# Kernel optimization log

Hardware: AMD Instinct MI355X
Metric: run time of the kernel (lower is better)

## Reference

```python
import jax, jax.numpy as jnp
import numpy as np

N_NODES = 100000
N_EDGES = 1600000
IN_FEAT = 128
HID_FEAT = 128
OUT_FEAT = 128


def setup_inputs() -> dict:
    key = jax.random.key(0)
    k1, k2, k3, k4, k5 = jax.random.split(key, 5)
    x = jax.random.normal(k1, (N_NODES, IN_FEAT), dtype=jnp.float32)
    # Xavier-ish scale for weights
    W_in = jax.random.normal(k2, (2, IN_FEAT, HID_FEAT), dtype=jnp.float32) * (1.0 / np.sqrt(IN_FEAT))
    W_out = jax.random.normal(k3, (2, HID_FEAT, OUT_FEAT), dtype=jnp.float32) * (1.0 / np.sqrt(HID_FEAT))
    src = jax.random.randint(k4, (N_EDGES,), 0, N_NODES, dtype=jnp.int32)
    dst = jax.random.randint(k5, (N_EDGES,), 0, N_NODES, dtype=jnp.int32)
    return {"x": x, "W_in": W_in, "W_out": W_out, "src": src, "dst": dst}


def _mean_aggregate(h, src, dst, num_nodes):
    # copy_src('h','m') + fn.mean('m','neigh'): gather src feats, segment-mean by dst.
    msgs = h[src]                                             # [E, D]
    summed = jax.ops.segment_sum(msgs, dst, num_segments=num_nodes)   # [N, D]
    deg = jax.ops.segment_sum(jnp.ones((src.shape[0],), h.dtype), dst,
                              num_segments=num_nodes)         # [N]
    deg = jnp.maximum(deg, 1.0)                               # zero-in-degree -> 0 output
    return summed / deg[:, None]


def reference(x, W_in, W_out, src, dst):
    n = x.shape[0]
    # Layer 0 (i == 0): uses weight_in, ReLU activation (i != K-1)
    neigh = _mean_aggregate(x, src, dst, n)
    h = x @ W_in[0] + neigh @ W_in[1]
    h = jax.nn.relu(h)
    # Layer 1 (i == K-1): uses weight_out, no activation
    neigh = _mean_aggregate(h, src, dst, n)
    h = h @ W_out[0] + neigh @ W_out[1]
    return h
```

## Files before the change

### kernel.cpp

```cpp
#include <hip/hip_runtime.h>

#define NF 128
#define NBSHIFT 8
#define NBMAX 512
#define CHUNK 4096

typedef __attribute__((ext_vector_type(8))) short bf16x8;
typedef __attribute__((ext_vector_type(4))) float f32x4;
typedef __attribute__((ext_vector_type(2))) float f32x2;

__device__ __forceinline__ unsigned short f2bf(float f) {
    unsigned int u = __builtin_bit_cast(unsigned int, f);
    u = (u + 0x7fffu + ((u >> 16) & 1u)) >> 16;
    return (unsigned short)u;
}
__device__ __forceinline__ float bflo(unsigned int u) {
    return __builtin_bit_cast(float, u << 16);
}
__device__ __forceinline__ float bfhi(unsigned int u) {
    return __builtin_bit_cast(float, u & 0xffff0000u);
}
__device__ __forceinline__ unsigned char f2fp8(float v) {
    return (unsigned char)(__builtin_amdgcn_cvt_pk_fp8_f32(v, v, 0, false) & 0xff);
}

#define BH 256
#define BT 256
__global__ __launch_bounds__(256) void k_prep(const int* __restrict__ dst, int E, int NB,
                                              int* __restrict__ gbhist,
                                              const float* __restrict__ x,
                                              unsigned short* __restrict__ xb,
                                              unsigned char* __restrict__ xq,
                                              const float* __restrict__ Win,
                                              const float* __restrict__ Wout,
                                              unsigned short* __restrict__ BtIn,
                                              unsigned short* __restrict__ BtOut) {
    __shared__ int lh[NBMAX];
    const int bb = blockIdx.x;
    const int t = threadIdx.x;
    if (bb < BH) {
        for (int k = t; k < NBMAX; k += 256) lh[k] = 0;
        __syncthreads();
        for (int i = bb * 256 + t; i < E; i += BH * 256)
            atomicAdd(&lh[((unsigned)dst[i]) >> NBSHIFT], 1);
        __syncthreads();
        for (int k = t; k < NB; k += 256)
            if (lh[k]) atomicAdd(&gbhist[k], lh[k]);
    } else if (bb < BH + BT) {
        int b2 = bb - BH;
        const float* W = (b2 < 128) ? Win : Wout;
        unsigned short* Bt = (b2 < 128) ? BtIn : BtOut;
        int idx = (b2 & 127) * 256 + t;
        int c = idx >> 8;
        int k = idx & 255;
        int p = k >> 7, kk = k & 127;
        Bt[idx] = f2bf(W[((size_t)p * NF + kk) * NF + c]);
    } else {
        long long i = (long long)(bb - BH - BT) * 256 + t;
        const float4 a = *reinterpret_cast<const float4*>(x + i * 8);
        const float4 b = *reinterpret_cast<const float4*>(x + i * 8 + 4);
        union { unsigned short s[8]; uint4 u; } o;
        o.s[0] = f2bf(a.x); o.s[1] = f2bf(a.y); o.s[2] = f2bf(a.z); o.s[3] = f2bf(a.w);
        o.s[4] = f2bf(b.x); o.s[5] = f2bf(b.y); o.s[6] = f2bf(b.z); o.s[7] = f2bf(b.w);
        *reinterpret_cast<uint4*>(xb + i * 8) = o.u;
        int lo = __builtin_amdgcn_cvt_pk_fp8_f32(a.x, a.y, 0, false);
        lo = __builtin_amdgcn_cvt_pk_fp8_f32(a.z, a.w, lo, true);
        int hi = __builtin_amdgcn_cvt_pk_fp8_f32(b.x, b.y, 0, false);
        hi = __builtin_amdgcn_cvt_pk_fp8_f32(b.z, b.w, hi, true);
        uint2 oq; oq.x = (unsigned)lo; oq.y = (unsigned)hi;
        *reinterpret_cast<uint2*>(xq + i * 8) = oq;
    }
}


__global__ __launch_bounds__(256) void k_bscan(const int* __restrict__ gbhist,
                                               int* __restrict__ bbase, int* __restrict__ gcursor,
                                               int NB, int E, int* __restrict__ offsets, int n) {
    __shared__ int sA[NBMAX], sB[NBMAX];
    int t = threadIdx.x;
    for (int k = t; k < NBMAX; k += 256) sA[k] = (k < NB) ? gbhist[k] : 0;
    __syncthreads();
    int* pin = sA;
    int* pout = sB;
    for (int off = 1; off < NBMAX; off <<= 1) {
        for (int k = t; k < NBMAX; k += 256) pout[k] = pin[k] + (k >= off ? pin[k - off] : 0);
        __syncthreads();
        int* tmp = pin; pin = pout; pout = tmp;
    }
    for (int k = t; k < NB; k += 256) {
        int excl = pin[k] - gbhist[k];
        bbase[k] = excl;
        gcursor[k] = excl;
    }
    if (t == 0) {
        bbase[NB] = E;
        offsets[n] = E;
    }
}

__global__ __launch_bounds__(256) void k_bucket(const int* __restrict__ src,
                                                const int* __restrict__ dst,
                                                int* __restrict__ gcursor,
                                                unsigned* __restrict__ gpairs, int E) {
    __shared__ int lhist[NBMAX], lbase[NBMAX], lcur[NBMAX], gb[NBMAX];
    __shared__ int sA[NBMAX], sB[NBMAX];
    __shared__ unsigned stage[CHUNK];
    __shared__ unsigned short stage_b[CHUNK];
    const int t = threadIdx.x;
    const int c0 = blockIdx.x * CHUNK;
    const int cc = min(CHUNK, E - c0);

    for (int k = t; k < NBMAX; k += 256) lhist[k] = 0;
    __syncthreads();

    int ls[16], ld[16];
#pragma unroll
    for (int j = 0; j < 16; ++j) {
        int i = t + j * 256;
        ls[j] = 0; ld[j] = 0;
        if (i < cc) {
            ls[j] = src[c0 + i];
            ld[j] = dst[c0 + i];
            atomicAdd(&lhist[((unsigned)ld[j]) >> NBSHIFT], 1);
        }
    }
    __syncthreads();
    for (int k = t; k < NBMAX; k += 256) sA[k] = lhist[k];
    __syncthreads();
    int* pin = sA;
    int* pout = sB;
    for (int off = 1; off < NBMAX; off <<= 1) {
        for (int k = t; k < NBMAX; k += 256) pout[k] = pin[k] + (k >= off ? pin[k - off] : 0);
        __syncthreads();
        int* tmp = pin; pin = pout; pout = tmp;
    }
    for (int k = t; k < NBMAX; k += 256) {
        int excl = pin[k] - lhist[k];
        lbase[k] = excl;
        lcur[k] = excl;
        int cnt = lhist[k];
        if (cnt > 0) gb[k] = atomicAdd(&gcursor[k], cnt);
    }
    __syncthreads();
#pragma unroll
    for (int j = 0; j < 16; ++j) {
        int i = t + j * 256;
        if (i < cc) {
            int b = ((unsigned)ld[j]) >> NBSHIFT;
            int pos = atomicAdd(&lcur[b], 1);
            stage[pos] = (((unsigned)ld[j] & 255u) << 24) | (unsigned)ls[j];
            stage_b[pos] = (unsigned short)b;
        }
    }
    __syncthreads();
    for (int idx = t; idx < cc; idx += 256) {
        unsigned p = stage[idx];
        int b = stage_b[idx];
        gpairs[gb[b] + (idx - lbase[b])] = p;
    }
}

__global__ __launch_bounds__(256) void k_bsort(const unsigned* __restrict__ gpairs,
                                               const int* __restrict__ bbase,
                                               int* __restrict__ offsets,
                                               float* __restrict__ invdeg,
                                               int* __restrict__ esrc, int n) {
    __shared__ int lcnt[256], lcur[256], sA[256], sB[256];
    const int b = blockIdx.x;
    const int t = threadIdx.x;
    const int base = bbase[b];
    const int c = bbase[b + 1] - base;
    const int n0 = b << NBSHIFT;

    lcnt[t] = 0;
    __syncthreads();
    for (int i = t; i < c; i += 256) {
        int node = (int)(gpairs[base + i] >> 24);
        atomicAdd(&lcnt[node], 1);
    }
    __syncthreads();
    sA[t] = lcnt[t];
    __syncthreads();
    int* pin = sA;
    int* pout = sB;
    for (int off = 1; off < 256; off <<= 1) {
        pout[t] = pin[t] + (t >= off ? pin[t - off] : 0);
        __syncthreads();
        int* tmp = pin; pin = pout; pout = tmp;
    }
    int excl = pin[t] - lcnt[t];
    lcur[t] = excl;
    int node_g = n0 + t;
    if (node_g < n) {
        offsets[node_g] = base + excl;
        invdeg[node_g] = 1.0f / (float)max(lcnt[t], 1);
    }
    __syncthreads();
    for (int i = t; i < c; i += 256) {
        unsigned p = gpairs[base + i];
        int node = (int)(p >> 24);
        int pos = atomicAdd(&lcur[node], 1);
        esrc[base + pos] = (int)(p & 0x00ffffffu);
    }
}

__global__ __launch_bounds__(256) void k_agg_fp8(const unsigned char* __restrict__ feat,
                                                 const int* __restrict__ esrc,
                                                 const int* __restrict__ offsets,
                                                 const float* __restrict__ invdeg,
                                                 unsigned short* __restrict__ neigh, int n) {
    int wid0 = (int)(((long long)blockIdx.x * blockDim.x + threadIdx.x) >> 6);
    const int wid = __builtin_amdgcn_readfirstlane(wid0);
    if (wid >= n) return;
    const int lane = threadIdx.x & 63;
    const int g = lane >> 4;
    const int q = lane & 15;
    const unsigned qoff = (unsigned)q * 8u;
    const unsigned char* fb = feat;

    const int beg = offsets[wid];
    const int end = offsets[wid + 1];
    f32x2 c01 = {0.f, 0.f}, c23 = {0.f, 0.f}, c45 = {0.f, 0.f}, c67 = {0.f, 0.f};

    int i = beg;
    for (; i + 16 <= end; i += 16) {
        int e[16];
#pragma unroll
        for (int j = 0; j < 16; ++j) e[j] = esrc[i + j];
#pragma unroll
        for (int u = 0; u < 4; ++u) {
            int es = (g & 2) ? ((g & 1) ? e[u * 4 + 3] : e[u * 4 + 2])
                             : ((g & 1) ? e[u * 4 + 1] : e[u * 4 + 0]);
            uint2 v = *(const uint2*)(fb + (unsigned)es * 128u + qoff);
            c01 += __builtin_amdgcn_cvt_pk_f32_fp8((int)v.x, false);
            c23 += __builtin_amdgcn_cvt_pk_f32_fp8((int)v.x, true);
            c45 += __builtin_amdgcn_cvt_pk_f32_fp8((int)v.y, false);
            c67 += __builtin_amdgcn_cvt_pk_f32_fp8((int)v.y, true);
        }
    }
    for (; i + 4 <= end; i += 4) {
        int e0 = esrc[i + 0], e1 = esrc[i + 1], e2 = esrc[i + 2], e3 = esrc[i + 3];
        int es = (g & 2) ? ((g & 1) ? e3 : e2) : ((g & 1) ? e1 : e0);
        uint2 v = *(const uint2*)(fb + (unsigned)es * 128u + qoff);
        c01 += __builtin_amdgcn_cvt_pk_f32_fp8((int)v.x, false);
        c23 += __builtin_amdgcn_cvt_pk_f32_fp8((int)v.x, true);
        c45 += __builtin_amdgcn_cvt_pk_f32_fp8((int)v.y, false);
        c67 += __builtin_amdgcn_cvt_pk_f32_fp8((int)v.y, true);
    }
    if (i < end) {
        int r = end - i;
        if (g < r) {
            int es = esrc[i + g];
            uint2 v = *(const uint2*)(fb + (unsigned)es * 128u + qoff);
            c01 += __builtin_amdgcn_cvt_pk_f32_fp8((int)v.x, false);
            c23 += __builtin_amdgcn_cvt_pk_f32_fp8((int)v.x, true);
            c45 += __builtin_amdgcn_cvt_pk_f32_fp8((int)v.y, false);
            c67 += __builtin_amdgcn_cvt_pk_f32_fp8((int)v.y, true);
        }
    }
    float a0 = c01.x, a1 = c01.y, a2 = c23.x, a3 = c23.y;
    float a4 = c45.x, a5 = c45.y, a6 = c67.x, a7 = c67.y;
    a0 += __shfl_xor(a0, 16); a1 += __shfl_xor(a1, 16);
    a2 += __shfl_xor(a2, 16); a3 += __shfl_xor(a3, 16);
    a4 += __shfl_xor(a4, 16); a5 += __shfl_xor(a5, 16);
    a6 += __shfl_xor(a6, 16); a7 += __shfl_xor(a7, 16);
    a0 += __shfl_xor(a0, 32); a1 += __shfl_xor(a1, 32);
    a2 += __shfl_xor(a2, 32); a3 += __shfl_xor(a3, 32);
    a4 += __shfl_xor(a4, 32); a5 += __shfl_xor(a5, 32);
    a6 += __shfl_xor(a6, 32); a7 += __shfl_xor(a7, 32);

    const float sc = invdeg[wid];
    a0 *= sc; a1 *= sc; a2 *= sc; a3 *= sc;
    a4 *= sc; a5 *= sc; a6 *= sc; a7 *= sc;
    unsigned p0, p1, p2, p3;
    asm("v_cvt_pk_bf16_f32 %0, %1, %2" : "=v"(p0) : "v"(a0), "v"(a1));
    asm("v_cvt_pk_bf16_f32 %0, %1, %2" : "=v"(p1) : "v"(a2), "v"(a3));
    asm("v_cvt_pk_bf16_f32 %0, %1, %2" : "=v"(p2) : "v"(a4), "v"(a5));
    asm("v_cvt_pk_bf16_f32 %0, %1, %2" : "=v"(p3) : "v"(a6), "v"(a7));
    if (g == 0) {
        uint4 o; o.x = p0; o.y = p1; o.z = p2; o.w = p3;
        *(uint4*)((char*)neigh + (size_t)wid * 256 + (unsigned)q * 16u) = o;
    }
}

__global__ __launch_bounds__(256) void k_agg_bf16(const unsigned short* __restrict__ feat,
                                                  const int* __restrict__ esrc,
                                                  const int* __restrict__ offsets,
                                                  const float* __restrict__ invdeg,
                                                  unsigned short* __restrict__ neigh, int n) {
    int wid0 = (int)(((long long)blockIdx.x * blockDim.x + threadIdx.x) >> 6);
    const int wid = __builtin_amdgcn_readfirstlane(wid0);
    if (wid >= n) return;
    const int lane = threadIdx.x & 63;
    const int g = lane >> 4;
    const int q = lane & 15;
    const unsigned qoff = (unsigned)q * 16u;
    const char* fb = (const char*)feat;
    const int beg = offsets[wid];
    const int end = offsets[wid + 1];
    float a0 = 0.f, a1 = 0.f, a2 = 0.f, a3 = 0.f, a4 = 0.f, a5 = 0.f, a6 = 0.f, a7 = 0.f;
    int i = beg;
    for (; i + 4 <= end; i += 4) {
        int e0 = esrc[i + 0], e1 = esrc[i + 1], e2 = esrc[i + 2], e3 = esrc[i + 3];
        int es = (g & 2) ? ((g & 1) ? e3 : e2) : ((g & 1) ? e1 : e0);
        uint4 v = *(const uint4*)(fb + (unsigned)es * 256u + qoff);
        a0 += bflo(v.x); a1 += bfhi(v.x);
        a2 += bflo(v.y); a3 += bfhi(v.y);
        a4 += bflo(v.z); a5 += bfhi(v.z);
        a6 += bflo(v.w); a7 += bfhi(v.w);
    }
    if (i < end) {
        int r = end - i;
        if (g < r) {
            int es = esrc[i + g];
            uint4 v = *(const uint4*)(fb + (unsigned)es * 256u + qoff);
            a0 += bflo(v.x); a1 += bfhi(v.x);
            a2 += bflo(v.y); a3 += bfhi(v.y);
            a4 += bflo(v.z); a5 += bfhi(v.z);
            a6 += bflo(v.w); a7 += bfhi(v.w);
        }
    }
    a0 += __shfl_xor(a0, 16); a1 += __shfl_xor(a1, 16);
    a2 += __shfl_xor(a2, 16); a3 += __shfl_xor(a3, 16);
    a4 += __shfl_xor(a4, 16); a5 += __shfl_xor(a5, 16);
    a6 += __shfl_xor(a6, 16); a7 += __shfl_xor(a7, 16);
    a0 += __shfl_xor(a0, 32); a1 += __shfl_xor(a1, 32);
    a2 += __shfl_xor(a2, 32); a3 += __shfl_xor(a3, 32);
    a4 += __shfl_xor(a4, 32); a5 += __shfl_xor(a5, 32);
    a6 += __shfl_xor(a6, 32); a7 += __shfl_xor(a7, 32);
    const float sc = invdeg[wid];
    a0 *= sc; a1 *= sc; a2 *= sc; a3 *= sc;
    a4 *= sc; a5 *= sc; a6 *= sc; a7 *= sc;
    unsigned p0, p1, p2, p3;
    asm("v_cvt_pk_bf16_f32 %0, %1, %2" : "=v"(p0) : "v"(a0), "v"(a1));
    asm("v_cvt_pk_bf16_f32 %0, %1, %2" : "=v"(p1) : "v"(a2), "v"(a3));
    asm("v_cvt_pk_bf16_f32 %0, %1, %2" : "=v"(p2) : "v"(a4), "v"(a5));
    asm("v_cvt_pk_bf16_f32 %0, %1, %2" : "=v"(p3) : "v"(a6), "v"(a7));
    if (g == 0) {
        uint4 o; o.x = p0; o.y = p1; o.z = p2; o.w = p3;
        *(uint4*)((char*)neigh + (size_t)wid * 256 + qoff) = o;
    }
}

__global__ __launch_bounds__(256) void k_agg_f32(const float* __restrict__ feat,
                                                 const int* __restrict__ esrc,
                                                 const int* __restrict__ offsets,
                                                 const float* __restrict__ invdeg,
                                                 unsigned short* __restrict__ neigh, int n) {
    int wid0 = (int)(((long long)blockIdx.x * blockDim.x + threadIdx.x) >> 6);
    const int wid = __builtin_amdgcn_readfirstlane(wid0);
    if (wid >= n) return;
    int lane = threadIdx.x & 63;
    int beg = offsets[wid], end = offsets[wid + 1];
    float a0 = 0.f, a1 = 0.f;
    for (int i = beg; i < end; ++i) {
        int s0 = esrc[i];
        float2 v0 = *(const float2*)(feat + (size_t)s0 * NF + lane * 2);
        a0 += v0.x; a1 += v0.y;
    }
    float sc = invdeg[wid];
    unsigned pk;
    float ca = a0 * sc, cb = a1 * sc;
    asm("v_cvt_pk_bf16_f32 %0, %1, %2" : "=v"(pk) : "v"(ca), "v"(cb));
    *(unsigned*)(neigh + (size_t)wid * NF + lane * 2) = pk;
}

template <bool RELU, bool A1BF16, bool OUTBF16, bool WRITEQ>
__global__ __launch_bounds__(256) void k_gemm_mfma(const void* __restrict__ A1v,
                                                   const unsigned short* __restrict__ A2,
                                                   const unsigned short* __restrict__ Bt,
                                                   void* __restrict__ outv,
                                                   unsigned char* __restrict__ outq,
                                                   int nrows) {
    const int tid = threadIdx.x;
    const int wave = tid >> 6;
    const int lane = tid & 63;
    const int l15 = lane & 15;
    const int lk = lane >> 4;
    const int col0 = wave * 32;
    const int rbase = blockIdx.x * 64;

    bf16x8 breg[2][8];
#pragma unroll
    for (int c = 0; c < 2; ++c)
#pragma unroll
        for (int kc = 0; kc < 8; ++kc)
            breg[c][kc] = *(const bf16x8*)(Bt + (size_t)(col0 + c * 16 + l15) * 256 +
                                           kc * 32 + lk * 8);

    f32x4 acc[4][2];
#pragma unroll
    for (int rc = 0; rc < 4; ++rc) {
        acc[rc][0] = (f32x4)0.0f;
        acc[rc][1] = (f32x4)0.0f;
    }

#pragma unroll
    for (int rc = 0; rc < 4; ++rc) {
        const int arow = rbase + rc * 16 + l15;
        const bool ok = arow < nrows;
        bf16x8 a[8];
        if (ok) {
            if (A1BF16) {
                const unsigned short* A1 = (const unsigned short*)A1v;
#pragma unroll
                for (int kc = 0; kc < 4; ++kc) {
                    a[kc] = *(const bf16x8*)(A1 + (size_t)arow * NF + kc * 32 + lk * 8);
                    a[kc + 4] = *(const bf16x8*)(A2 + (size_t)arow * NF + kc * 32 + lk * 8);
                }
            } else {
                const float* A1 = (const float*)A1v;
#pragma unroll
                for (int kc = 0; kc < 4; ++kc) {
                    const float* p = A1 + (size_t)arow * NF + kc * 32 + lk * 8;
                    float4 u = *(const float4*)p;
                    float4 v = *(const float4*)(p + 4);
                    a[kc][0] = (short)f2bf(u.x); a[kc][1] = (short)f2bf(u.y);
                    a[kc][2] = (short)f2bf(u.z); a[kc][3] = (short)f2bf(u.w);
                    a[kc][4] = (short)f2bf(v.x); a[kc][5] = (short)f2bf(v.y);
                    a[kc][6] = (short)f2bf(v.z); a[kc][7] = (short)f2bf(v.w);
                    a[kc + 4] = *(const bf16x8*)(A2 + (size_t)arow * NF + kc * 32 + lk * 8);
                }
            }
        } else {
#pragma unroll
            for (int kc = 0; kc < 8; ++kc) a[kc] = (bf16x8)(short)0;
        }
#pragma unroll
        for (int kc = 0; kc < 8; ++kc) {
            acc[rc][0] = __builtin_amdgcn_mfma_f32_16x16x32_bf16(a[kc], breg[0][kc],
                                                                 acc[rc][0], 0, 0, 0);
            acc[rc][1] = __builtin_amdgcn_mfma_f32_16x16x32_bf16(a[kc], breg[1][kc],
                                                                 acc[rc][1], 0, 0, 0);
        }
    }

#pragma unroll
    for (int rc = 0; rc < 4; ++rc) {
#pragma unroll
        for (int r = 0; r < 4; ++r) {
            const int orow = rbase + rc * 16 + lk * 4 + r;
            if (orow >= nrows) continue;
#pragma unroll
            for (int c = 0; c < 2; ++c) {
                float v = acc[rc][c][r];
                if (RELU) v = fmaxf(v, 0.f);
                const int col = col0 + c * 16 + l15;
                if (OUTBF16)
                    ((unsigned short*)outv)[(size_t)orow * NF + col] = f2bf(v);
                else
                    ((float*)outv)[(size_t)orow * NF + col] = v;
                if (WRITEQ)
                    outq[(size_t)orow * NF + col] = f2fp8(v);
            }
        }
    }
}

extern "C" void kernel_launch(void* const* d_in, const int* in_sizes, int n_in,
                              void* d_out, int out_size, void* d_ws, size_t ws_size,
                              hipStream_t stream) {
    const float* x = (const float*)d_in[0];
    const float* W_in = (const float*)d_in[1];
    const float* W_out = (const float*)d_in[2];
    const int* src = (const int*)d_in[3];
    const int* dst = (const int*)d_in[4];

    const int n = in_sizes[0] / NF;
    const int E = in_sizes[3];
    float* outp = (float*)d_out;

    const int NB = (n + 255) >> NBSHIFT;
    const int nchunks = (E + CHUNK - 1) / CHUNK;

    char* ws = (char*)d_ws;
    size_t off = 0;
    auto take = [&](size_t bytes) {
        void* p = ws + off;
        off = (off + bytes + 511) & ~(size_t)511;
        return p;
    };
    int* gbhist = (int*)take((size_t)NB * 4);
    int* bbase = (int*)take((size_t)(NB + 1) * 4);
    int* gcursor = (int*)take((size_t)NB * 4);
    int* offsets = (int*)take((size_t)(n + 1) * 4);
    float* invdeg = (float*)take((size_t)n * 4);
    unsigned short* BtIn = (unsigned short*)take(128 * 256 * 2);
    unsigned short* BtOut = (unsigned short*)take(128 * 256 * 2);
    unsigned* gpairs = (unsigned*)take((size_t)E * 4);
    int* esrc = (int*)take((size_t)E * 4);
    unsigned short* hb = (unsigned short*)take((size_t)n * NF * 2);
    unsigned short* neigh = (unsigned short*)take((size_t)n * NF * 2);
    size_t need_fp8 = off + (size_t)n * NF * 2 + 512 + (size_t)n * NF + 512 +
                      (size_t)n * NF + 512;
    bool use_fp8 = (ws_size >= need_fp8);
    unsigned short* xb = nullptr;
    unsigned char* xq = nullptr;
    unsigned char* hq = nullptr;
    if (use_fp8) {
        xb = (unsigned short*)take((size_t)n * NF * 2);
        xq = (unsigned char*)take((size_t)n * NF);
        hq = (unsigned char*)take((size_t)n * NF);
    }
    bool use_xb = use_fp8 || (ws_size >= off + (size_t)n * NF * 2);
    if (!use_fp8 && use_xb) xb = (unsigned short*)take((size_t)n * NF * 2);

    hipMemsetAsync(gbhist, 0, (size_t)NB * 4, stream);
    const int cvtBlocks = use_fp8 ? (int)(((long long)n * NF / 8 + 255) / 256) : 0;
    k_prep<<<BH + BT + cvtBlocks, 256, 0, stream>>>(dst, E, NB, gbhist, x, xb, xq,
                                                    W_in, W_out, BtIn, BtOut);
    k_bscan<<<1, 256, 0, stream>>>(gbhist, bbase, gcursor, NB, E, offsets, n);
    k_bucket<<<nchunks, 256, 0, stream>>>(src, dst, gcursor, gpairs, E);
    k_bsort<<<NB, 256, 0, stream>>>(gpairs, bbase, offsets, invdeg, esrc, n);

    const int aggBlocks = (n + 3) / 4;
    const int gemmBlocks = (n + 63) / 64;

    if (use_fp8) {
        k_agg_fp8<<<aggBlocks, 256, 0, stream>>>(xq, esrc, offsets, invdeg, neigh, n);
        k_gemm_mfma<true, true, true, true>
            <<<gemmBlocks, 256, 0, stream>>>(xb, neigh, BtIn, hb, hq, n);
        k_agg_fp8<<<aggBlocks, 256, 0, stream>>>(hq, esrc, offsets, invdeg, neigh, n);
        k_gemm_mfma<false, true, false, false>
            <<<gemmBlocks, 256, 0, stream>>>(hb, neigh, BtOut, outp, nullptr, n);
    } else {
        k_agg_f32<<<aggBlocks, 256, 0, stream>>>(x, esrc, offsets, invdeg, neigh, n);
        k_gemm_mfma<true, false, true, false>
            <<<gemmBlocks, 256, 0, stream>>>(x, neigh, BtIn, hb, nullptr, n);
        k_agg_bf16<<<aggBlocks, 256, 0, stream>>>(hb, esrc, offsets, invdeg, neigh, n);
        k_gemm_mfma<false, true, false, false>
            <<<gemmBlocks, 256, 0, stream>>>(hb, neigh, BtOut, outp, nullptr, n);
    }
}
```

Measured before the change: 240.0 us.

## Stage GEMM A tiles through LDS and coalesce output stores via shared memory

Adds a new GEMM kernel for the fp8 path. It loads the 64-row bf16 A tiles (self and neighbour features) into XOR-swizzled LDS using direct global-to-LDS loads, then feeds the MFMA from LDS. The results are staged back through LDS so the bf16, fp8 and fp32 outputs are written with 16-byte coalesced stores instead of scattered 2- and 4-byte stores. This adds barriers and 32 KB of LDS per block, which may lower occupancy.

```diff
diff --git a/kernel.cpp b/kernel.cpp
--- a/kernel.cpp
+++ b/kernel.cpp
@@ -365,13 +365,137 @@
     *(unsigned*)(neigh + (size_t)wid * NF + lane * 2) = pk;
 }
 
-template <bool RELU, bool A1BF16, bool OUTBF16, bool WRITEQ>
+template <bool RELU, bool OUTBF16, bool WRITEQ>
+__global__ __launch_bounds__(256) void k_gemm_lds(const unsigned short* __restrict__ A1,
+                                                  const unsigned short* __restrict__ A2,
+                                                  const unsigned short* __restrict__ Bt,
+                                                  void* __restrict__ outv,
+                                                  unsigned char* __restrict__ outq,
+                                                  int nrows) {
+    __shared__ __align__(16) unsigned char sm[32768];
+    const int tid = threadIdx.x;
+    const int w = tid >> 6;
+    const int lane = tid & 63;
+    const int l15 = lane & 15;
+    const int lk = lane >> 4;
+    const int col0 = w * 32;
+    const int rbase = blockIdx.x * 64;
+
+#pragma unroll
+    for (int h = 0; h < 2; ++h) {
+        const unsigned short* Ah = h ? A2 : A1;
+#pragma unroll
+        for (int j = 0; j < 4; ++j) {
+            const int r = w * 16 + j * 4 + lk;
+            const int garow = min(rbase + r, nrows - 1);
+            const int cch = l15 ^ (r & 7);
+            const unsigned short* srcp = Ah + (size_t)garow * NF + cch * 8;
+            unsigned char* ldst = &sm[h * 16384 + (w * 16 + j * 4) * 256];
+            __builtin_amdgcn_global_load_lds(
+                (const __attribute__((address_space(1))) void*)srcp,
+                (__attribute__((address_space(3))) void*)ldst, 16, 0, 0);
+        }
+    }
+
+    bf16x8 breg[2][8];
+#pragma unroll
+    for (int c = 0; c < 2; ++c)
+#pragma unroll
+        for (int kc = 0; kc < 8; ++kc)
+            breg[c][kc] = *(const bf16x8*)(Bt + (size_t)(col0 + c * 16 + l15) * 256 +
+                                           kc * 32 + lk * 8);
+
+    f32x4 acc[4][2];
+#pragma unroll
+    for (int rc = 0; rc < 4; ++rc) {
+        acc[rc][0] = (f32x4)0.0f;
+        acc[rc][1] = (f32x4)0.0f;
+    }
+
+    __syncthreads();
+
+#pragma unroll
+    for (int rc = 0; rc < 4; ++rc) {
+        const int row = rc * 16 + l15;
+#pragma unroll
+        for (int kc = 0; kc < 8; ++kc) {
+            const int half = kc >> 2;
+            const int kk = kc & 3;
+            const int chunk = (kk * 4 + lk) ^ (row & 7);
+            const bf16x8 a = *(const bf16x8*)&sm[half * 16384 + row * 256 + chunk * 16];
+            acc[rc][0] = __builtin_amdgcn_mfma_f32_16x16x32_bf16(a, breg[0][kc],
+                                                                 acc[rc][0], 0, 0, 0);
+            acc[rc][1] = __builtin_amdgcn_mfma_f32_16x16x32_bf16(a, breg[1][kc],
+                                                                 acc[rc][1], 0, 0, 0);
+        }
+    }
+
+    __syncthreads();
+
+    if (OUTBF16) {
+        unsigned short* smb = (unsigned short*)sm;
+        unsigned char* smq = sm + 16384;
+#pragma unroll
+        for (int rc = 0; rc < 4; ++rc)
+#pragma unroll
+            for (int r = 0; r < 4; ++r) {
+                const int row = rc * 16 + lk * 4 + r;
+#pragma unroll
+                for (int c = 0; c < 2; ++c) {
+                    float v = acc[rc][c][r];
+                    if (RELU) v = fmaxf(v, 0.f);
+                    const int col = col0 + c * 16 + l15;
+                    smb[row * NF + col] = f2bf(v);
+                    if (WRITEQ) smq[row * NF + col] = f2fp8(v);
+                }
+            }
+        __syncthreads();
+#pragma unroll
+        for (int it = 0; it < 4; ++it) {
+            const int off = (tid + it * 256) * 16;
+            if (rbase + (off >> 8) < nrows)
+                *(uint4*)((char*)outv + (size_t)rbase * 256 + off) =
+                    *(const uint4*)&sm[off];
+        }
+        if (WRITEQ) {
+#pragma unroll
+            for (int it = 0; it < 2; ++it) {
+                const int off = (tid + it * 256) * 16;
+                if (rbase + (off >> 7) < nrows)
+                    *(uint4*)(outq + (size_t)rbase * 128 + off) =
+                        *(const uint4*)&sm[16384 + off];
+            }
+        }
+    } else {
+        float* smf = (float*)sm;
+#pragma unroll
+        for (int rc = 0; rc < 4; ++rc)
+#pragma unroll
+            for (int r = 0; r < 4; ++r) {
+                const int row = rc * 16 + lk * 4 + r;
+#pragma unroll
+                for (int c = 0; c < 2; ++c) {
+                    float v = acc[rc][c][r];
+                    if (RELU) v = fmaxf(v, 0.f);
+                    smf[row * NF + col0 + c * 16 + l15] = v;
+                }
+            }
+        __syncthreads();
+#pragma unroll
+        for (int it = 0; it < 8; ++it) {
+            const int off = (tid + it * 256) * 16;
+            if (rbase + (off >> 9) < nrows)
+                *(uint4*)((char*)outv + (size_t)rbase * 512 + off) =
+                    *(const uint4*)&sm[off];
+        }
+    }
+}
+
+template <bool RELU, bool A1BF16, bool OUTBF16>
 __global__ __launch_bounds__(256) void k_gemm_mfma(const void* __restrict__ A1v,
                                                    const unsigned short* __restrict__ A2,
                                                    const unsigned short* __restrict__ Bt,
-                                                   void* __restrict__ outv,
-                                                   unsigned char* __restrict__ outq,
-                                                   int nrows) {
+                                                   void* __restrict__ outv, int nrows) {
     const int tid = threadIdx.x;
     const int wave = tid >> 6;
     const int lane = tid & 63;
@@ -450,8 +574,6 @@
                     ((unsigned short*)outv)[(size_t)orow * NF + col] = f2bf(v);
                 else
                     ((float*)outv)[(size_t)orow * NF + col] = v;
-                if (WRITEQ)
-                    outq[(size_t)orow * NF + col] = f2fp8(v);
             }
         }
     }
@@ -518,17 +640,17 @@
 
     if (use_fp8) {
         k_agg_fp8<<<aggBlocks, 256, 0, stream>>>(xq, esrc, offsets, invdeg, neigh, n);
-        k_gemm_mfma<true, true, true, true>
+        k_gemm_lds<true, true, true>
             <<<gemmBlocks, 256, 0, stream>>>(xb, neigh, BtIn, hb, hq, n);
         k_agg_fp8<<<aggBlocks, 256, 0, stream>>>(hq, esrc, offsets, invdeg, neigh, n);
-        k_gemm_mfma<false, true, false, false>
+        k_gemm_lds<false, false, false>
             <<<gemmBlocks, 256, 0, stream>>>(hb, neigh, BtOut, outp, nullptr, n);
     } else {
         k_agg_f32<<<aggBlocks, 256, 0, stream>>>(x, esrc, offsets, invdeg, neigh, n);
-        k_gemm_mfma<true, false, true, false>
-            <<<gemmBlocks, 256, 0, stream>>>(x, neigh, BtIn, hb, nullptr, n);
+        k_gemm_mfma<true, false, true>
+            <<<gemmBlocks, 256, 0, stream>>>(x, neigh, BtIn, hb, n);
         k_agg_bf16<<<aggBlocks, 256, 0, stream>>>(hb, esrc, offsets, invdeg, neigh, n);
-        k_gemm_mfma<false, true, false, false>
-            <<<gemmBlocks, 256, 0, stream>>>(hb, neigh, BtOut, outp, nullptr, n);
-    }
-}
+        k_gemm_mfma<false, true, false>
+            <<<gemmBlocks, 256, 0, stream>>>(hb, neigh, BtOut, outp, n);
+    }
+}
```

New measurement: 198.3 us. 17.4% less time.
